# Performance work log

Measured on AMD Instinct MI355X. Metric: run time of the kernel, lower is better.

## Reference

```python
import jax, jax.numpy as jnp
import numpy as np

N = 100000   # nodes
E = 800000   # directed edges
IN = 256     # in_channels (== hidden, required by repo's vn MLP dims)
HID = 256    # hidden_channels
OUT = 40     # out_channels (arxiv classes)
EPS = 1e-5


def setup_inputs() -> dict:
    key = jax.random.key(0)
    ks = jax.random.split(key, 8)
    def nrm(k, shape, scale=0.05):
        return jax.random.normal(k, shape, dtype=jnp.float32) * scale
    return {
        "x": nrm(ks[0], (N, IN), 1.0),
        "edge_index": jax.random.randint(ks[1], (2, E), 0, N, dtype=jnp.int32),
        # GCNConv weights (PyG: x @ W, then normalized aggregation, then + bias)
        "W0": nrm(ks[2], (IN, HID)),  "b0": jnp.zeros((HID,), jnp.float32),
        "W1": nrm(ks[3], (HID, HID)), "b1": jnp.zeros((HID,), jnp.float32),
        "W2": nrm(ks[4], (HID, OUT)), "b2": jnp.zeros((OUT,), jnp.float32),
        # BatchNorm1d affine params (batch-stat math, training mode)
        "bn_g0": jnp.ones((HID,), jnp.float32), "bn_b0": jnp.zeros((HID,), jnp.float32),
        "bn_g1": jnp.ones((HID,), jnp.float32), "bn_b1": jnp.zeros((HID,), jnp.float32),
        # virtual node embedding (init to 0 per reset_parameters)
        "vn_emb": jnp.zeros((1, IN), jnp.float32),
        # mlp_vns[0]: Linear(IN,HID) + LayerNorm(HID) + ReLU
        "vn_W0": nrm(ks[5], (IN, HID)),  "vn_b0": jnp.zeros((HID,), jnp.float32),
        "ln_g0": jnp.ones((HID,), jnp.float32), "ln_b0": jnp.zeros((HID,), jnp.float32),
        # mlp_vns[1]: Linear(HID,HID) + LayerNorm(HID) + ReLU
        "vn_W1": nrm(ks[6], (HID, HID)), "vn_b1": jnp.zeros((HID,), jnp.float32),
        "ln_g1": jnp.ones((HID,), jnp.float32), "ln_b1": jnp.zeros((HID,), jnp.float32),
    }


def _forward(x, edge_index, W0, b0, W1, b1, W2, b2, bn_g0, bn_b0, bn_g1, bn_b1,
             vn_emb, vn_W0, vn_b0, ln_g0, ln_b0, vn_W1, vn_b1, ln_g1, ln_b1):
    src, dst = edge_index[0], edge_index[1]
    # GCN symmetric normalization with self-loops: deg = in-degree + 1
    deg = jax.ops.segment_sum(jnp.ones(src.shape, jnp.float32), dst, num_segments=N) + 1.0
    dis = jax.lax.rsqrt(deg)                       # deg^{-1/2}  [N]
    coef = (dis[src] * dis[dst])[:, None]          # edge norm   [E,1]
    self_coef = (dis * dis)[:, None]               # self-loop norm = deg^{-1}  [N,1]

    def gcn(h, W, b):
        h = h @ W                                             # [N, out]
        agg = jax.ops.segment_sum(h[src] * coef, dst, num_segments=N)
        return agg + h * self_coef + b

    def bn(h, g, bv):  # BatchNorm1d, batch statistics over nodes
        mu = h.mean(0)
        var = ((h - mu) ** 2).mean(0)
        return (h - mu) * jax.lax.rsqrt(var + EPS) * g + bv

    def ln(h, g, bv):  # LayerNorm over last dim
        mu = h.mean(-1, keepdims=True)
        var = ((h - mu) ** 2).mean(-1, keepdims=True)
        return (h - mu) * jax.lax.rsqrt(var + EPS) * g + bv

    vx = vn_emb                                   # [1, IN]
    # layer 0
    h = x + vx                                    # virtual-node broadcast
    h = gcn(h, W0, b0)
    h = jax.nn.relu(bn(h, bn_g0, bn_b0))          # dropout = identity (eval)
    pool = jnp.sum(h, axis=0, keepdims=True)      # global_add_pool
    vx = jax.nn.relu(ln((pool + vx) @ vn_W0 + vn_b0, ln_g0, ln_b0))
    # layer 1
    h = h + vx
    h = gcn(h, W1, b1)
    h = jax.nn.relu(bn(h, bn_g1, bn_b1))
    pool = jnp.sum(h, axis=0, keepdims=True)
    vx = jax.nn.relu(ln((pool + vx) @ vn_W1 + vn_b1, ln_g1, ln_b1))
    # layer 2 (output)
    h = h + vx
    h = gcn(h, W2, b2)
    return jax.nn.log_softmax(h, axis=-1)


def reference(x, edge_index, W0, b0, W1, b1, W2, b2, bn_g0, bn_b0, bn_g1, bn_b1,
              vn_emb, vn_W0, vn_b0, ln_g0, ln_b0, vn_W1, vn_b1, ln_g1, ln_b1):
    return _forward(x, edge_index, W0, b0, W1, b1, W2, b2, bn_g0, bn_b0, bn_g1, bn_b1,
                    vn_emb, vn_W0, vn_b0, ln_g0, ln_b0, vn_W1, vn_b1, ln_g1, ln_b1)
```

## Files before the change

kernel.cpp:

```cpp
#include <hip/hip_runtime.h>
#include <hip/hip_bf16.h>
#include <cstdint>

#define N_NODES 100000
#define N_EDGES 800000
#define CH      256
#define COUT    40
#define COUTP   48
#define EPS     1e-5f
#define SCAN_CHUNK 1024
#define NSCAN_BLK  98
#define AGG_NPW 16
#define AGG_BLOCKS 2048
#define AGG_WAVES  (AGG_BLOCKS * 4)

typedef unsigned short u16;
typedef unsigned int   u32;
typedef short s16x8 __attribute__((ext_vector_type(8)));
typedef float f32x4 __attribute__((ext_vector_type(4)));

__device__ __forceinline__ float b2f(u32 u) { return __uint_as_float(u << 16); }
__device__ __forceinline__ u16 f2b(float f) {
    u32 u = __float_as_uint(f);
    u32 r = (u + 0x7fffu + ((u >> 16) & 1u)) >> 16;
    return (u16)r;
}
__device__ __forceinline__ u32 packb(float a, float b) {
    return (u32)f2b(a) | ((u32)f2b(b) << 16);
}
__device__ __forceinline__ void unpack8(uint4 v, float* f) {
    f[0] = b2f(v.x & 0xffffu); f[1] = b2f(v.x >> 16);
    f[2] = b2f(v.y & 0xffffu); f[3] = b2f(v.y >> 16);
    f[4] = b2f(v.z & 0xffffu); f[5] = b2f(v.z >> 16);
    f[6] = b2f(v.w & 0xffffu); f[7] = b2f(v.w >> 16);
}

__global__ void k_count(const int* __restrict__ dst, int* __restrict__ counts) {
    int e = blockIdx.x * 256 + threadIdx.x;
    if (e < N_EDGES) atomicAdd(&counts[dst[e]], 1);
}

__global__ void k_scan1(const int* __restrict__ counts, int* __restrict__ partial,
                        int* __restrict__ blocksums) {
    __shared__ int sdata[256];
    int base = blockIdx.x * SCAN_CHUNK;
    int t = threadIdx.x;
    int v[4]; int s = 0;
    for (int j = 0; j < 4; j++) {
        int i = base + t * 4 + j;
        v[j] = (i < N_NODES) ? counts[i] : 0;
        s += v[j];
    }
    sdata[t] = s; __syncthreads();
    for (int off = 1; off < 256; off <<= 1) {
        int x = (t >= off) ? sdata[t - off] : 0;
        __syncthreads();
        sdata[t] += x;
        __syncthreads();
    }
    int incl = sdata[t];
    int run = incl - s;
    if (t == 255) blocksums[blockIdx.x] = incl;
    for (int j = 0; j < 4; j++) {
        int i = base + t * 4 + j;
        if (i < N_NODES) partial[i] = run;
        run += v[j];
    }
}

__global__ void k_scan3(int* __restrict__ row_start, const int* __restrict__ blocksums,
                        int* __restrict__ cursor, const int* __restrict__ counts,
                        float* __restrict__ dis) {
    __shared__ int sd[128], raw[128];
    int t = threadIdx.x;
    if (t < 128) {
        int v = (t < NSCAN_BLK) ? blocksums[t] : 0;
        sd[t] = v; raw[t] = v;
    }
    __syncthreads();
    for (int off = 1; off < 128; off <<= 1) {
        int x = (t < 128 && t >= off) ? sd[t - off] : 0;
        __syncthreads();
        if (t < 128) sd[t] += x;
        __syncthreads();
    }
    int i = blockIdx.x * 256 + t;
    if (i < N_NODES) {
        int j = i >> 10;
        int v = row_start[i] + (sd[j] - raw[j]);
        row_start[i] = v;
        cursor[i] = v;
        dis[i] = rsqrtf(1.0f + (float)counts[i]);
    }
}

__global__ void k_fill(const int* __restrict__ src, const int* __restrict__ dst,
                       int* __restrict__ cursor, int2* __restrict__ edata,
                       const float* __restrict__ dis) {
    int e = blockIdx.x * 256 + threadIdx.x;
    if (e < N_EDGES) {
        int d = dst[e], s = src[e];
        int p = atomicAdd(&cursor[d], 1);
        int2 v; v.x = s; v.y = __float_as_int(dis[s] * dis[d]);
        edata[p] = v;
    }
}

#define PREP_ZBASE (513 + COUTP)
#define PREP_ZN    (N_NODES + 2560 + 2560)
#define PREP_BLOCKS (PREP_ZBASE + (PREP_ZN + 255) / 256)
__global__ void k_prep(const float* __restrict__ W0, const float* __restrict__ W1,
                       const float* __restrict__ W2,
                       u16* __restrict__ T0, u16* __restrict__ T1, u16* __restrict__ T2,
                       const float* __restrict__ vec, float* __restrict__ v20,
                       int* __restrict__ counts, float* __restrict__ statsA,
                       float* __restrict__ statsB) {
    __shared__ float s[256];
    int b = blockIdx.x, t = threadIdx.x;
    if (b < 256) {
        T0[b * 256 + t] = f2b(W0[t * 256 + b]);
    } else if (b < 512) {
        int n = b - 256;
        T1[n * 256 + t] = f2b(W1[t * 256 + n]);
    } else if (b < 512 + COUTP) {
        int n = b - 512;
        T2[n * 256 + t] = f2b(n < COUT ? W2[t * COUT + n] : 0.f);
    } else if (b == 512 + COUTP) {
        s[t] = vec[t];
        __syncthreads();
        float acc = 0.f;
        for (int k = 0; k < 256; k++) acc += s[k] * W0[k * 256 + t];
        v20[t] = acc;
    } else {
        int idx = (b - PREP_ZBASE) * 256 + t;
        if (idx < N_NODES) counts[idx] = 0;
        else if ((idx -= N_NODES) < 2560) statsA[idx] = 0.f;
        else if ((idx -= 2560) < 2560) statsB[idx] = 0.f;
    }
}

__global__ __launch_bounds__(512) void k_gemm_f32a(const float* __restrict__ A,
                                                   const u16* __restrict__ Wt,
                                                   u16* __restrict__ Hout) {
    __shared__ u16 Bs[256 * 72];
    __shared__ u16 As[128 * 72];
    const int t = threadIdx.x;
    const int wave = t >> 6, lane = t & 63;
    const int lm = lane & 15, quad = lane >> 4;
    const int wr = wave & 1, wc = wave >> 1;
    const int m0 = blockIdx.x * 128;
    const int ar = t >> 2, as_ = (t & 3) * 16;
    const int arow = m0 + ar;
    const int brow = t >> 1, bo = (t & 1) * 32;
    const f32x4 vz = {0.f, 0.f, 0.f, 0.f};
    f32x4 acc[4][4];
    for (int m = 0; m < 4; m++)
        for (int c = 0; c < 4; c++) acc[m][c] = vz;

    for (int k0 = 0; k0 < 256; k0 += 64) {
        {
            const uint4* bsrc = (const uint4*)(Wt + brow * 256 + k0 + bo);
            uint4* bdst = (uint4*)(Bs + brow * 72 + bo);
#pragma unroll
            for (int j = 0; j < 4; j++) bdst[j] = bsrc[j];
            uint4 p0 = {0,0,0,0}, p1 = {0,0,0,0};
            if (arow < N_NODES) {
                const float4* asrc = (const float4*)(A + (size_t)arow * 256 + k0 + as_);
                float4 x0 = asrc[0], x1 = asrc[1], x2 = asrc[2], x3 = asrc[3];
                p0.x = packb(x0.x, x0.y); p0.y = packb(x0.z, x0.w);
                p0.z = packb(x1.x, x1.y); p0.w = packb(x1.z, x1.w);
                p1.x = packb(x2.x, x2.y); p1.y = packb(x2.z, x2.w);
                p1.z = packb(x3.x, x3.y); p1.w = packb(x3.z, x3.w);
            }
            uint4* adst = (uint4*)(As + ar * 72 + as_);
            adst[0] = p0; adst[1] = p1;
        }
        __syncthreads();
#pragma unroll
        for (int kk = 0; kk < 64; kk += 32) {
            s16x8 af[4], bf[4];
#pragma unroll
            for (int m = 0; m < 4; m++)
                af[m] = *(const s16x8*)(As + (wr * 64 + m * 16 + lm) * 72 + kk + quad * 8);
#pragma unroll
            for (int c = 0; c < 4; c++)
                bf[c] = *(const s16x8*)(Bs + (wc * 64 + c * 16 + lm) * 72 + kk + quad * 8);
#pragma unroll
            for (int c = 0; c < 4; c++)
#pragma unroll
                for (int m = 0; m < 4; m++)
                    acc[m][c] = __builtin_amdgcn_mfma_f32_16x16x32_bf16(af[m], bf[c], acc[m][c], 0, 0, 0);
        }
        __syncthreads();
    }
#pragma unroll
    for (int m = 0; m < 4; m++) {
#pragma unroll
        for (int c = 0; c < 4; c++) {
            int col = wc * 64 + c * 16 + lm;
#pragma unroll
            for (int i = 0; i < 4; i++) {
                int row = m0 + wr * 64 + m * 16 + quad * 4 + i;
                if (row < N_NODES) Hout[(size_t)row * 256 + col] = f2b(acc[m][c][i]);
            }
        }
    }
}

__global__ __launch_bounds__(512) void k_gemm_bn(const u16* __restrict__ A,
                                                 const float* __restrict__ stats,
                                                 const float* __restrict__ g,
                                                 const float* __restrict__ bv,
                                                 const u16* __restrict__ Wt,
                                                 u16* __restrict__ Hout,
                                                 float* __restrict__ pool) {
    __shared__ u16 Bs[256 * 72];
    __shared__ u16 As[128 * 72];
    __shared__ float ggs[256], bcs[256], pls[256];
    const int t = threadIdx.x;
    const int wave = t >> 6, lane = t & 63;
    const int lm = lane & 15, quad = lane >> 4;
    const int wr = wave & 1, wc = wave >> 1;
    const int m0 = blockIdx.x * 128;
    const int ar = t >> 2, as_ = (t & 3) * 16;
    const int arow = m0 + ar;
    const int brow = t >> 1, bo = (t & 1) * 32;
    if (t < 256) {
        const float inv = 1.0f / (float)N_NODES;
        float mu = stats[t] * inv;
        float var = stats[256 + t] * inv - mu * mu;
        float rs = rsqrtf(var + EPS);
        float gg = g[t] * rs;
        ggs[t] = gg; bcs[t] = bv[t] - mu * gg;
        pls[t] = 0.f;
    }
    __syncthreads();
    const f32x4 vz = {0.f, 0.f, 0.f, 0.f};
    f32x4 acc[4][4];
    for (int m = 0; m < 4; m++)
        for (int c = 0; c < 4; c++) acc[m][c] = vz;

    for (int k0 = 0; k0 < 256; k0 += 64) {
        {
            const uint4* bsrc = (const uint4*)(Wt + brow * 256 + k0 + bo);
            uint4* bdst = (uint4*)(Bs + brow * 72 + bo);
#pragma unroll
            for (int j = 0; j < 4; j++) bdst[j] = bsrc[j];
            float f[16];
            if (arow < N_NODES) {
                const uint4* asrc = (const uint4*)(A + (size_t)arow * 256 + k0 + as_);
                uint4 r0 = asrc[0], r1 = asrc[1];
                unpack8(r0, f); unpack8(r1, f + 8);
#pragma unroll
                for (int j = 0; j < 16; j++) {
                    int c = k0 + as_ + j;
                    f[j] = fmaxf(f[j] * ggs[c] + bcs[c], 0.f);
                }
            } else {
#pragma unroll
                for (int j = 0; j < 16; j++) f[j] = 0.f;
            }
#pragma unroll
            for (int j = 0; j < 16; j++) {
                float v = f[j];
                v += __shfl_xor(v, 4);  v += __shfl_xor(v, 8);
                v += __shfl_xor(v, 16); v += __shfl_xor(v, 32);
                if (lane < 4) atomicAdd(&pls[k0 + lane * 16 + j], v);
            }
            uint4 p0, p1;
            p0.x = packb(f[0], f[1]);   p0.y = packb(f[2], f[3]);
            p0.z = packb(f[4], f[5]);   p0.w = packb(f[6], f[7]);
            p1.x = packb(f[8], f[9]);   p1.y = packb(f[10], f[11]);
            p1.z = packb(f[12], f[13]); p1.w = packb(f[14], f[15]);
            uint4* adst = (uint4*)(As + ar * 72 + as_);
            adst[0] = p0; adst[1] = p1;
        }
        __syncthreads();
#pragma unroll
        for (int kk = 0; kk < 64; kk += 32) {
            s16x8 af[4], bf[4];
#pragma unroll
            for (int m = 0; m < 4; m++)
                af[m] = *(const s16x8*)(As + (wr * 64 + m * 16 + lm) * 72 + kk + quad * 8);
#pragma unroll
            for (int c = 0; c < 4; c++)
                bf[c] = *(const s16x8*)(Bs + (wc * 64 + c * 16 + lm) * 72 + kk + quad * 8);
#pragma unroll
            for (int c = 0; c < 4; c++)
#pragma unroll
                for (int m = 0; m < 4; m++)
                    acc[m][c] = __builtin_amdgcn_mfma_f32_16x16x32_bf16(af[m], bf[c], acc[m][c], 0, 0, 0);
        }
        __syncthreads();
    }
    if (t < 256) atomicAdd(&pool[(blockIdx.x & 7) * 256 + t], pls[t]);
#pragma unroll
    for (int m = 0; m < 4; m++) {
#pragma unroll
        for (int c = 0; c < 4; c++) {
            int col = wc * 64 + c * 16 + lm;
#pragma unroll
            for (int i = 0; i < 4; i++) {
                int row = m0 + wr * 64 + m * 16 + quad * 4 + i;
                if (row < N_NODES) Hout[(size_t)row * 256 + col] = f2b(acc[m][c][i]);
            }
        }
    }
}

__global__ __launch_bounds__(512) void k_gemm2_bn(const u16* __restrict__ A,
                                                  const float* __restrict__ stats,
                                                  const float* __restrict__ g,
                                                  const float* __restrict__ bv,
                                                  const u16* __restrict__ Wt,
                                                  u16* __restrict__ Hout,
                                                  float* __restrict__ pool) {
    __shared__ u16 Bs[48 * 72];
    __shared__ u16 As[128 * 72];
    __shared__ float ggs[256], bcs[256], pls[256];
    const int t = threadIdx.x;
    const int wave = t >> 6, lane = t & 63;
    const int lm = lane & 15, quad = lane >> 4;
    const int m0 = blockIdx.x * 128;
    const int ar = t >> 2, as_ = (t & 3) * 16;
    const int arow = m0 + ar;
    if (t < 256) {
        const float inv = 1.0f / (float)N_NODES;
        float mu = stats[t] * inv;
        float var = stats[256 + t] * inv - mu * mu;
        float rs = rsqrtf(var + EPS);
        float gg = g[t] * rs;
        ggs[t] = gg; bcs[t] = bv[t] - mu * gg;
        pls[t] = 0.f;
    }
    __syncthreads();
    const f32x4 vz = {0.f, 0.f, 0.f, 0.f};
    f32x4 acc[3]; acc[0] = vz; acc[1] = vz; acc[2] = vz;

    for (int k0 = 0; k0 < 256; k0 += 64) {
        {
            if (t < 48) {
                const uint4* bsrc = (const uint4*)(Wt + t * 256 + k0);
                uint4* bdst = (uint4*)(Bs + t * 72);
#pragma unroll
                for (int j = 0; j < 8; j++) bdst[j] = bsrc[j];
            }
            float f[16];
            if (arow < N_NODES) {
                const uint4* asrc = (const uint4*)(A + (size_t)arow * 256 + k0 + as_);
                uint4 r0 = asrc[0], r1 = asrc[1];
                unpack8(r0, f); unpack8(r1, f + 8);
#pragma unroll
                for (int j = 0; j < 16; j++) {
                    int c = k0 + as_ + j;
                    f[j] = fmaxf(f[j] * ggs[c] + bcs[c], 0.f);
                }
            } else {
#pragma unroll
                for (int j = 0; j < 16; j++) f[j] = 0.f;
            }
#pragma unroll
            for (int j = 0; j < 16; j++) {
                float v = f[j];
                v += __shfl_xor(v, 4);  v += __shfl_xor(v, 8);
                v += __shfl_xor(v, 16); v += __shfl_xor(v, 32);
                if (lane < 4) atomicAdd(&pls[k0 + lane * 16 + j], v);
            }
            uint4 p0, p1;
            p0.x = packb(f[0], f[1]);   p0.y = packb(f[2], f[3]);
            p0.z = packb(f[4], f[5]);   p0.w = packb(f[6], f[7]);
            p1.x = packb(f[8], f[9]);   p1.y = packb(f[10], f[11]);
            p1.z = packb(f[12], f[13]); p1.w = packb(f[14], f[15]);
            uint4* adst = (uint4*)(As + ar * 72 + as_);
            adst[0] = p0; adst[1] = p1;
        }
        __syncthreads();
#pragma unroll
        for (int kk = 0; kk < 64; kk += 32) {
            s16x8 af = *(const s16x8*)(As + (wave * 16 + lm) * 72 + kk + quad * 8);
#pragma unroll
            for (int c = 0; c < 3; c++) {
                s16x8 bf = *(const s16x8*)(Bs + (c * 16 + lm) * 72 + kk + quad * 8);
                acc[c] = __builtin_amdgcn_mfma_f32_16x16x32_bf16(af, bf, acc[c], 0, 0, 0);
            }
        }
        __syncthreads();
    }
    if (t < 256) atomicAdd(&pool[(blockIdx.x & 7) * 256 + t], pls[t]);
#pragma unroll
    for (int c = 0; c < 3; c++) {
        int col = c * 16 + lm;
#pragma unroll
        for (int i = 0; i < 4; i++) {
            int row = m0 + wave * 16 + quad * 4 + i;
            if (row < N_NODES) Hout[(size_t)row * COUTP + col] = f2b(acc[c][i]);
        }
    }
}

__global__ __launch_bounds__(256) void k_agg(const u16* __restrict__ H2,
                                             const int* __restrict__ row_start,
                                             const int* __restrict__ counts,
                                             const int2* __restrict__ edata,
                                             const float* __restrict__ dis,
                                             const float* __restrict__ bias,
                                             const float* __restrict__ v2,
                                             u16* __restrict__ OutB,
                                             float* __restrict__ stats) {
    __shared__ float ls[512];
    const int t = threadIdx.x, wave = t >> 6, lane = t & 63;
    const int half = lane >> 5, hl = lane & 31;
    const int ci = hl * 8;
    const float4 bbA = *(const float4*)(bias + ci);
    const float4 bbB = *(const float4*)(bias + ci + 4);
    const float4 vvA = *(const float4*)(v2 + ci);
    const float4 vvB = *(const float4*)(v2 + ci + 4);
    float s[8], q[8];
#pragma unroll
    for (int j = 0; j < 8; j++) { s[j] = 0.f; q[j] = 0.f; }

    const int gwave = blockIdx.x * 4 + wave;
    const int nid = gwave + lane * AGG_WAVES;
    const bool nv = (lane < AGG_NPW) && (nid < N_NODES);
    const int   my_rs = nv ? row_start[nid] : 0;
    const int   my_ct = nv ? counts[nid] : 0;
    const float my_dn = nv ? dis[nid] : 0.f;

    int beg = __shfl(my_rs, 0), cnt = __shfl(my_ct, 0);
    int2 my_e = {0, 0};
    if (lane < cnt) my_e = edata[beg + lane];

    for (int i = 0; i < AGG_NPW; i++) {
        const int node = gwave + i * AGG_WAVES;
        if (node >= N_NODES) break;
        const int2 cur_e = my_e;
        const int  ccnt = cnt, cbeg = beg;
        const float dn = __shfl(my_dn, i);
        const uint4 rs_ = *(const uint4*)(H2 + (size_t)node * 256 + ci);
        if (i + 1 < AGG_NPW && node + AGG_WAVES < N_NODES) {
            beg = __shfl(my_rs, i + 1);
            cnt = __shfl(my_ct, i + 1);
            int2 tmp = {0, 0};
            if (lane < cnt) tmp = edata[beg + lane];
            my_e = tmp;
        }
        const int cnt64 = ccnt < 64 ? ccnt : 64;
        const int cnt8 = (cnt64 + 7) & ~7;
        float a[8];
#pragma unroll
        for (int j = 0; j < 8; j++) a[j] = 0.f;
        float cs = 0.f;
        for (int e = 0; e < cnt8; e += 8) {
            const int   si0 = __shfl(cur_e.x, e + half);
            const int   si1 = __shfl(cur_e.x, e + 2 + half);
            const int   si2 = __shfl(cur_e.x, e + 4 + half);
            const int   si3 = __shfl(cur_e.x, e + 6 + half);
            const float cf0 = __int_as_float(__shfl(cur_e.y, e + half));
            const float cf1 = __int_as_float(__shfl(cur_e.y, e + 2 + half));
            const float cf2 = __int_as_float(__shfl(cur_e.y, e + 4 + half));
            const float cf3 = __int_as_float(__shfl(cur_e.y, e + 6 + half));
            const uint4 r0 = *(const uint4*)(H2 + (size_t)si0 * 256 + ci);
            const uint4 r1 = *(const uint4*)(H2 + (size_t)si1 * 256 + ci);
            const uint4 r2 = *(const uint4*)(H2 + (size_t)si2 * 256 + ci);
            const uint4 r3 = *(const uint4*)(H2 + (size_t)si3 * 256 + ci);
            cs += cf0 + cf1 + cf2 + cf3;
            a[0] += cf0*b2f(r0.x&0xffffu) + cf1*b2f(r1.x&0xffffu) + cf2*b2f(r2.x&0xffffu) + cf3*b2f(r3.x&0xffffu);
            a[1] += cf0*b2f(r0.x>>16)     + cf1*b2f(r1.x>>16)     + cf2*b2f(r2.x>>16)     + cf3*b2f(r3.x>>16);
            a[2] += cf0*b2f(r0.y&0xffffu) + cf1*b2f(r1.y&0xffffu) + cf2*b2f(r2.y&0xffffu) + cf3*b2f(r3.y&0xffffu);
            a[3] += cf0*b2f(r0.y>>16)     + cf1*b2f(r1.y>>16)     + cf2*b2f(r2.y>>16)     + cf3*b2f(r3.y>>16);
            a[4] += cf0*b2f(r0.z&0xffffu) + cf1*b2f(r1.z&0xffffu) + cf2*b2f(r2.z&0xffffu) + cf3*b2f(r3.z&0xffffu);
            a[5] += cf0*b2f(r0.z>>16)     + cf1*b2f(r1.z>>16)     + cf2*b2f(r2.z>>16)     + cf3*b2f(r3.z>>16);
            a[6] += cf0*b2f(r0.w&0xffffu) + cf1*b2f(r1.w&0xffffu) + cf2*b2f(r2.w&0xffffu) + cf3*b2f(r3.w&0xffffu);
            a[7] += cf0*b2f(r0.w>>16)     + cf1*b2f(r1.w>>16)     + cf2*b2f(r2.w>>16)     + cf3*b2f(r3.w>>16);
        }
        if (ccnt > 64) {
            int e2 = 64;
            for (; e2 + 2 <= ccnt; e2 += 2) {
                const int2 ed_ = edata[cbeg + e2 + half];
                const float cf = __int_as_float(ed_.y);
                const uint4 r = *(const uint4*)(H2 + (size_t)ed_.x * 256 + ci);
                cs += cf;
                a[0] += cf*b2f(r.x&0xffffu); a[1] += cf*b2f(r.x>>16);
                a[2] += cf*b2f(r.y&0xffffu); a[3] += cf*b2f(r.y>>16);
                a[4] += cf*b2f(r.z&0xffffu); a[5] += cf*b2f(r.z>>16);
                a[6] += cf*b2f(r.w&0xffffu); a[7] += cf*b2f(r.w>>16);
            }
            if (e2 < ccnt && half == 0) {
                const int2 ed_ = edata[cbeg + e2];
                const float cf = __int_as_float(ed_.y);
                const uint4 r = *(const uint4*)(H2 + (size_t)ed_.x * 256 + ci);
                cs += cf;
                a[0] += cf*b2f(r.x&0xffffu); a[1] += cf*b2f(r.x>>16);
                a[2] += cf*b2f(r.y&0xffffu); a[3] += cf*b2f(r.y>>16);
                a[4] += cf*b2f(r.z&0xffffu); a[5] += cf*b2f(r.z>>16);
                a[6] += cf*b2f(r.w&0xffffu); a[7] += cf*b2f(r.w>>16);
            }
        }
        cs += __shfl_xor(cs, 32);
#pragma unroll
        for (int j = 0; j < 8; j++) a[j] += __shfl_xor(a[j], 32);
        const float sc = dn * dn, cv = cs + sc;
        const float f0 = a[0] + sc*b2f(rs_.x&0xffffu) + cv*vvA.x + bbA.x;
        const float f1 = a[1] + sc*b2f(rs_.x>>16)     + cv*vvA.y + bbA.y;
        const float f2 = a[2] + sc*b2f(rs_.y&0xffffu) + cv*vvA.z + bbA.z;
        const float f3 = a[3] + sc*b2f(rs_.y>>16)     + cv*vvA.w + bbA.w;
        const float f4 = a[4] + sc*b2f(rs_.z&0xffffu) + cv*vvB.x + bbB.x;
        const float f5 = a[5] + sc*b2f(rs_.z>>16)     + cv*vvB.y + bbB.y;
        const float f6 = a[6] + sc*b2f(rs_.w&0xffffu) + cv*vvB.z + bbB.z;
        const float f7 = a[7] + sc*b2f(rs_.w>>16)     + cv*vvB.w + bbB.w;
        if (half == 0) {
            uint4 o;
            o.x = packb(f0, f1); o.y = packb(f2, f3);
            o.z = packb(f4, f5); o.w = packb(f6, f7);
            *(uint4*)(OutB + (size_t)node * 256 + ci) = o;
        }
        s[0] += f0; q[0] += f0*f0;  s[1] += f1; q[1] += f1*f1;
        s[2] += f2; q[2] += f2*f2;  s[3] += f3; q[3] += f3*f3;
        s[4] += f4; q[4] += f4*f4;  s[5] += f5; q[5] += f5*f5;
        s[6] += f6; q[6] += f6*f6;  s[7] += f7; q[7] += f7*f7;
    }
    ls[t] = 0.f; ls[256 + t] = 0.f;
    __syncthreads();
    if (half == 0) {
#pragma unroll
        for (int j = 0; j < 8; j++) {
            atomicAdd(&ls[ci + j], s[j]);
            atomicAdd(&ls[256 + ci + j], q[j]);
        }
    }
    __syncthreads();
    atomicAdd(&stats[t], ls[t]);
    atomicAdd(&stats[256 + t], ls[256 + t]);
}

__global__ void k_vx(const float* __restrict__ pool, const float* __restrict__ vx_old,
                     const float* __restrict__ vnW, const float* __restrict__ vnb,
                     const float* __restrict__ lng, const float* __restrict__ lnb,
                     float* __restrict__ vx_new,
                     const float* __restrict__ Wnext, int ncn, int npn,
                     float* __restrict__ v2n) {
    __shared__ float s[256];
    __shared__ float red[256];
    int t = threadIdx.x;
    float pv = 0.f;
#pragma unroll
    for (int r = 0; r < 8; r++) pv += pool[r * 256 + t];
    s[t] = pv + vx_old[t];
    __syncthreads();
    float y = vnb[t];
    for (int k = 0; k < 256; k++) y += s[k] * vnW[k * 256 + t];
    red[t] = y; __syncthreads();
    for (int off = 128; off > 0; off >>= 1) {
        if (t < off) red[t] += red[t + off];
        __syncthreads();
    }
    float mu = red[0] * (1.f / 256.f);
    __syncthreads();
    float d = y - mu;
    red[t] = d * d; __syncthreads();
    for (int off = 128; off > 0; off >>= 1) {
        if (t < off) red[t] += red[t + off];
        __syncthreads();
    }
    float var = red[0] * (1.f / 256.f);
    float v = fmaxf(d * rsqrtf(var + EPS) * lng[t] + lnb[t], 0.f);
    vx_new[t] = v;
    __syncthreads();
    s[t] = v;
    __syncthreads();
    float acc = 0.f;
    if (t < ncn) {
        for (int k = 0; k < 256; k++) acc += s[k] * Wnext[k * ncn + t];
    }
    if (t < npn) v2n[t] = acc;
}

__global__ __launch_bounds__(256) void k_agg2(const u16* __restrict__ H2,
                                              const int* __restrict__ row_start,
                                              const int* __restrict__ counts,
                                              const int2* __restrict__ edata,
                                              const float* __restrict__ dis,
                                              const float* __restrict__ bias,
                                              const float* __restrict__ v2,
                                              float* __restrict__ OutF) {
    const int t = threadIdx.x, wave = t >> 6, lane = t & 63;
    const int half = lane >> 5, hl = lane & 31;
    const bool gact = hl < 24;
    const bool cact = hl < 20;
    const int c0 = 2 * hl;
    float bb0 = 0.f, bb1 = 0.f, vv0 = 0.f, vv1 = 0.f;
    if (cact) {
        float2 bv = *(const float2*)(bias + c0); bb0 = bv.x; bb1 = bv.y;
        float2 vvv = *(const float2*)(v2 + c0);  vv0 = vvv.x; vv1 = vvv.y;
    }
    const int nbase = blockIdx.x * 16 + wave * 4;
    for (int i = 0; i < 4; i++) {
        const int node = nbase + i;
        const int beg = row_start[node], cnt = counts[node];
        const float dn = dis[node];
        float a0 = 0.f, a1 = 0.f, cs = 0.f;
        int e = half;
        for (; e + 6 < cnt; e += 8) {
            int2 ea = edata[beg+e],   eb = edata[beg+e+2];
            int2 ec = edata[beg+e+4], ed = edata[beg+e+6];
            float ca = __int_as_float(ea.y), cb = __int_as_float(eb.y);
            float cc = __int_as_float(ec.y), cd = __int_as_float(ed.y);
            u32 ra = 0, rb = 0, rc = 0, rd = 0;
            if (gact) {
                ra = *(const u32*)(H2 + (size_t)ea.x * COUTP + c0);
                rb = *(const u32*)(H2 + (size_t)eb.x * COUTP + c0);
                rc = *(const u32*)(H2 + (size_t)ec.x * COUTP + c0);
                rd = *(const u32*)(H2 + (size_t)ed.x * COUTP + c0);
            }
            cs += ca + cb + cc + cd;
            a0 += ca*b2f(ra&0xffffu) + cb*b2f(rb&0xffffu) + cc*b2f(rc&0xffffu) + cd*b2f(rd&0xffffu);
            a1 += ca*b2f(ra>>16)     + cb*b2f(rb>>16)     + cc*b2f(rc>>16)     + cd*b2f(rd>>16);
        }
        for (; e < cnt; e += 2) {
            int2 ea = edata[beg+e];
            float ca = __int_as_float(ea.y);
            u32 ra = gact ? *(const u32*)(H2 + (size_t)ea.x * COUTP + c0) : 0u;
            cs += ca;
            a0 += ca*b2f(ra&0xffffu); a1 += ca*b2f(ra>>16);
        }
        a0 += __shfl_xor(a0, 32);
        a1 += __shfl_xor(a1, 32);
        cs += __shfl_xor(cs, 32);
        const float sc = dn * dn;
        u32 rs_ = gact ? *(const u32*)(H2 + (size_t)node * COUTP + c0) : 0u;
        float h0 = a0 + sc*b2f(rs_&0xffffu) + (cs+sc)*vv0 + bb0;
        float h1 = a1 + sc*b2f(rs_>>16)     + (cs+sc)*vv1 + bb1;
        float m = cact ? fmaxf(h0, h1) : -3.0e38f;
#pragma unroll
        for (int off = 16; off > 0; off >>= 1) m = fmaxf(m, __shfl_xor(m, off));
        float ex = cact ? (expf(h0 - m) + expf(h1 - m)) : 0.f;
        float se = ex;
#pragma unroll
        for (int off = 16; off > 0; off >>= 1) se += __shfl_xor(se, off);
        float lg = logf(se);
        if (cact && half == 0) {
            float2 o = {h0 - m - lg, h1 - m - lg};
            *(float2*)(OutF + (size_t)node * COUT + c0) = o;
        }
    }
}

extern "C" void kernel_launch(void* const* d_in, const int* in_sizes, int n_in,
                              void* d_out, int out_size, void* d_ws, size_t ws_size,
                              hipStream_t stream) {
    const float* x   = (const float*)d_in[0];
    const int*   ei  = (const int*)d_in[1];
    const int*   esrc = ei;
    const int*   edst = ei + N_EDGES;
    const float* W0 = (const float*)d_in[2];  const float* b0 = (const float*)d_in[3];
    const float* W1 = (const float*)d_in[4];  const float* b1 = (const float*)d_in[5];
    const float* W2 = (const float*)d_in[6];  const float* b2 = (const float*)d_in[7];
    const float* bg0 = (const float*)d_in[8]; const float* bb0 = (const float*)d_in[9];
    const float* bg1 = (const float*)d_in[10]; const float* bb1 = (const float*)d_in[11];
    const float* vn_emb = (const float*)d_in[12];
    const float* vW0 = (const float*)d_in[13]; const float* vb0 = (const float*)d_in[14];
    const float* lg0 = (const float*)d_in[15]; const float* lb0 = (const float*)d_in[16];
    const float* vW1 = (const float*)d_in[17]; const float* vb1 = (const float*)d_in[18];
    const float* lg1 = (const float*)d_in[19]; const float* lb1 = (const float*)d_in[20];

    char* w = (char*)d_ws;
    auto alloc = [&](size_t bytes) { void* p = (void*)w; w += ((bytes + 255) / 256) * 256; return p; };
    u16* H2    = (u16*)alloc((size_t)N_NODES * 256 * 2);
    u16* OutB  = (u16*)alloc((size_t)N_NODES * 256 * 2);
    int2* edata = (int2*)alloc((size_t)N_EDGES * 8);
    int* counts = (int*)alloc((size_t)N_NODES * 4);
    int* rowst  = (int*)alloc((size_t)N_NODES * 4);
    int* cursor = (int*)alloc((size_t)N_NODES * 4);
    float* dis  = (float*)alloc((size_t)N_NODES * 4);
    u16* Wtb0 = (u16*)alloc(256 * 256 * 2);
    u16* Wtb1 = (u16*)alloc(256 * 256 * 2);
    u16* Wt2b = (u16*)alloc(COUTP * 256 * 2);
    int* scanblk = (int*)alloc(128 * 4);
    float* statsA = (float*)alloc(2560 * 4);
    float* statsB = (float*)alloc(2560 * 4);
    float* vxA = (float*)alloc(256 * 4);
    float* vxB = (float*)alloc(256 * 4);
    float* v20 = (float*)alloc(256 * 4);
    float* v21 = (float*)alloc(256 * 4);
    float* v22 = (float*)alloc(64 * 4);
    (void)ws_size; (void)in_sizes; (void)n_in; (void)out_size;

    k_prep<<<PREP_BLOCKS, 256, 0, stream>>>(W0, W1, W2, Wtb0, Wtb1, Wt2b,
                                            vn_emb, v20, counts, statsA, statsB);
    k_count<<<(N_EDGES + 255) / 256, 256, 0, stream>>>(edst, counts);
    k_scan1<<<NSCAN_BLK, 256, 0, stream>>>(counts, rowst, scanblk);
    k_scan3<<<(N_NODES + 255) / 256, 256, 0, stream>>>(rowst, scanblk, cursor, counts, dis);
    k_fill<<<(N_EDGES + 255) / 256, 256, 0, stream>>>(esrc, edst, cursor, edata, dis);

    const int gemmblk = (N_NODES + 127) / 128;

    k_gemm_f32a<<<gemmblk, 512, 0, stream>>>(x, Wtb0, H2);
    k_agg<<<AGG_BLOCKS, 256, 0, stream>>>(H2, rowst, counts, edata, dis, b0, v20, OutB, statsA);
    k_gemm_bn<<<gemmblk, 512, 0, stream>>>(OutB, statsA, bg0, bb0, Wtb1, H2, statsA + 512);
    k_vx<<<1, 256, 0, stream>>>(statsA + 512, vn_emb, vW0, vb0, lg0, lb0, vxA, W1, 256, 256, v21);
    k_agg<<<AGG_BLOCKS, 256, 0, stream>>>(H2, rowst, counts, edata, dis, b1, v21, OutB, statsB);
    k_gemm2_bn<<<gemmblk, 512, 0, stream>>>(OutB, statsB, bg1, bb1, Wt2b, H2, statsB + 512);
    k_vx<<<1, 256, 0, stream>>>(statsB + 512, vxA, vW1, vb1, lg1, lb1, vxB, W2, COUT, COUTP, v22);
    k_agg2<<<N_NODES / 16, 256, 0, stream>>>(H2, rowst, counts, edata, dis, b2, v22, (float*)d_out);
}
```

Measured before the change: 719.4 us.

## Load GEMM B fragments directly from global memory instead of staging in LDS

The three GEMM kernels no longer copy the transposed weight tile into shared memory each k-step. Each lane now reads its B fragment straight from global memory, relying on cache hits since the weights are small and shared by every block. This removes the LDS stores and frees shared memory, which may raise occupancy, at the cost of more global/L2 traffic per MFMA. The padded output width grows from 48 to 64 to match four 16-column MFMA tiles, and the final aggregation only loads the 40 real columns.

```diff
diff --git a/kernel.cpp b/kernel.cpp
--- a/kernel.cpp
+++ b/kernel.cpp
@@ -6,7 +6,7 @@
 #define N_EDGES 800000
 #define CH      256
 #define COUT    40
-#define COUTP   48
+#define COUTP   64
 #define EPS     1e-5f
 #define SCAN_CHUNK 1024
 #define NSCAN_BLK  98
@@ -142,7 +142,6 @@
 __global__ __launch_bounds__(512) void k_gemm_f32a(const float* __restrict__ A,
                                                    const u16* __restrict__ Wt,
                                                    u16* __restrict__ Hout) {
-    __shared__ u16 Bs[256 * 72];
     __shared__ u16 As[128 * 72];
     const int t = threadIdx.x;
     const int wave = t >> 6, lane = t & 63;
@@ -151,7 +150,7 @@
     const int m0 = blockIdx.x * 128;
     const int ar = t >> 2, as_ = (t & 3) * 16;
     const int arow = m0 + ar;
-    const int brow = t >> 1, bo = (t & 1) * 32;
+    const u16* bbase = Wt + (wc * 64 + lm) * 256 + quad * 8;
     const f32x4 vz = {0.f, 0.f, 0.f, 0.f};
     f32x4 acc[4][4];
     for (int m = 0; m < 4; m++)
@@ -159,10 +158,6 @@
 
     for (int k0 = 0; k0 < 256; k0 += 64) {
         {
-            const uint4* bsrc = (const uint4*)(Wt + brow * 256 + k0 + bo);
-            uint4* bdst = (uint4*)(Bs + brow * 72 + bo);
-#pragma unroll
-            for (int j = 0; j < 4; j++) bdst[j] = bsrc[j];
             uint4 p0 = {0,0,0,0}, p1 = {0,0,0,0};
             if (arow < N_NODES) {
                 const float4* asrc = (const float4*)(A + (size_t)arow * 256 + k0 + as_);
@@ -184,7 +179,7 @@
                 af[m] = *(const s16x8*)(As + (wr * 64 + m * 16 + lm) * 72 + kk + quad * 8);
 #pragma unroll
             for (int c = 0; c < 4; c++)
-                bf[c] = *(const s16x8*)(Bs + (wc * 64 + c * 16 + lm) * 72 + kk + quad * 8);
+                bf[c] = *(const s16x8*)(bbase + c * 16 * 256 + k0 + kk);
 #pragma unroll
             for (int c = 0; c < 4; c++)
 #pragma unroll
@@ -214,7 +209,6 @@
                                                  const u16* __restrict__ Wt,
                                                  u16* __restrict__ Hout,
                                                  float* __restrict__ pool) {
-    __shared__ u16 Bs[256 * 72];
     __shared__ u16 As[128 * 72];
     __shared__ float ggs[256], bcs[256], pls[256];
     const int t = threadIdx.x;
@@ -224,7 +218,7 @@
     const int m0 = blockIdx.x * 128;
     const int ar = t >> 2, as_ = (t & 3) * 16;
     const int arow = m0 + ar;
-    const int brow = t >> 1, bo = (t & 1) * 32;
+    const u16* bbase = Wt + (wc * 64 + lm) * 256 + quad * 8;
     if (t < 256) {
         const float inv = 1.0f / (float)N_NODES;
         float mu = stats[t] * inv;
@@ -242,10 +236,6 @@
 
     for (int k0 = 0; k0 < 256; k0 += 64) {
         {
-            const uint4* bsrc = (const uint4*)(Wt + brow * 256 + k0 + bo);
-            uint4* bdst = (uint4*)(Bs + brow * 72 + bo);
-#pragma unroll
-            for (int j = 0; j < 4; j++) bdst[j] = bsrc[j];
             float f[16];
             if (arow < N_NODES) {
                 const uint4* asrc = (const uint4*)(A + (size_t)arow * 256 + k0 + as_);
@@ -284,7 +274,7 @@
                 af[m] = *(const s16x8*)(As + (wr * 64 + m * 16 + lm) * 72 + kk + quad * 8);
 #pragma unroll
             for (int c = 0; c < 4; c++)
-                bf[c] = *(const s16x8*)(Bs + (wc * 64 + c * 16 + lm) * 72 + kk + quad * 8);
+                bf[c] = *(const s16x8*)(bbase + c * 16 * 256 + k0 + kk);
 #pragma unroll
             for (int c = 0; c < 4; c++)
 #pragma unroll
@@ -315,7 +305,6 @@
                                                   const u16* __restrict__ Wt,
                                                   u16* __restrict__ Hout,
                                                   float* __restrict__ pool) {
-    __shared__ u16 Bs[48 * 72];
     __shared__ u16 As[128 * 72];
     __shared__ float ggs[256], bcs[256], pls[256];
     const int t = threadIdx.x;
@@ -324,6 +313,7 @@
     const int m0 = blockIdx.x * 128;
     const int ar = t >> 2, as_ = (t & 3) * 16;
     const int arow = m0 + ar;
+    const u16* bbase = Wt + lm * 256 + quad * 8;
     if (t < 256) {
         const float inv = 1.0f / (float)N_NODES;
         float mu = stats[t] * inv;
@@ -335,16 +325,10 @@
     }
     __syncthreads();
     const f32x4 vz = {0.f, 0.f, 0.f, 0.f};
-    f32x4 acc[3]; acc[0] = vz; acc[1] = vz; acc[2] = vz;
+    f32x4 acc[4]; acc[0] = vz; acc[1] = vz; acc[2] = vz; acc[3] = vz;
 
     for (int k0 = 0; k0 < 256; k0 += 64) {
         {
-            if (t < 48) {
-                const uint4* bsrc = (const uint4*)(Wt + t * 256 + k0);
-                uint4* bdst = (uint4*)(Bs + t * 72);
-#pragma unroll
-                for (int j = 0; j < 8; j++) bdst[j] = bsrc[j];
-            }
             float f[16];
             if (arow < N_NODES) {
                 const uint4* asrc = (const uint4*)(A + (size_t)arow * 256 + k0 + as_);
@@ -379,8 +363,8 @@
         for (int kk = 0; kk < 64; kk += 32) {
             s16x8 af = *(const s16x8*)(As + (wave * 16 + lm) * 72 + kk + quad * 8);
 #pragma unroll
-            for (int c = 0; c < 3; c++) {
-                s16x8 bf = *(const s16x8*)(Bs + (c * 16 + lm) * 72 + kk + quad * 8);
+            for (int c = 0; c < 4; c++) {
+                s16x8 bf = *(const s16x8*)(bbase + c * 16 * 256 + k0 + kk);
                 acc[c] = __builtin_amdgcn_mfma_f32_16x16x32_bf16(af, bf, acc[c], 0, 0, 0);
             }
         }
@@ -388,7 +372,7 @@
     }
     if (t < 256) atomicAdd(&pool[(blockIdx.x & 7) * 256 + t], pls[t]);
 #pragma unroll
-    for (int c = 0; c < 3; c++) {
+    for (int c = 0; c < 4; c++) {
         int col = c * 16 + lm;
 #pragma unroll
         for (int i = 0; i < 4; i++) {
@@ -585,7 +569,6 @@
                                               float* __restrict__ OutF) {
     const int t = threadIdx.x, wave = t >> 6, lane = t & 63;
     const int half = lane >> 5, hl = lane & 31;
-    const bool gact = hl < 24;
     const bool cact = hl < 20;
     const int c0 = 2 * hl;
     float bb0 = 0.f, bb1 = 0.f, vv0 = 0.f, vv1 = 0.f;
@@ -606,7 +589,7 @@
             float ca = __int_as_float(ea.y), cb = __int_as_float(eb.y);
             float cc = __int_as_float(ec.y), cd = __int_as_float(ed.y);
             u32 ra = 0, rb = 0, rc = 0, rd = 0;
-            if (gact) {
+            if (cact) {
                 ra = *(const u32*)(H2 + (size_t)ea.x * COUTP + c0);
                 rb = *(const u32*)(H2 + (size_t)eb.x * COUTP + c0);
                 rc = *(const u32*)(H2 + (size_t)ec.x * COUTP + c0);
@@ -619,7 +602,7 @@
         for (; e < cnt; e += 2) {
             int2 ea = edata[beg+e];
             float ca = __int_as_float(ea.y);
-            u32 ra = gact ? *(const u32*)(H2 + (size_t)ea.x * COUTP + c0) : 0u;
+            u32 ra = cact ? *(const u32*)(H2 + (size_t)ea.x * COUTP + c0) : 0u;
             cs += ca;
             a0 += ca*b2f(ra&0xffffu); a1 += ca*b2f(ra>>16);
         }
@@ -627,7 +610,7 @@
         a1 += __shfl_xor(a1, 32);
         cs += __shfl_xor(cs, 32);
         const float sc = dn * dn;
-        u32 rs_ = gact ? *(const u32*)(H2 + (size_t)node * COUTP + c0) : 0u;
+        u32 rs_ = cact ? *(const u32*)(H2 + (size_t)node * COUTP + c0) : 0u;
         float h0 = a0 + sc*b2f(rs_&0xffffu) + (cs+sc)*vv0 + bb0;
         float h1 = a1 + sc*b2f(rs_>>16)     + (cs+sc)*vv1 + bb1;
         float m = cact ? fmaxf(h0, h1) : -3.0e38f;
@@ -682,7 +665,7 @@
     float* vxB = (float*)alloc(256 * 4);
     float* v20 = (float*)alloc(256 * 4);
     float* v21 = (float*)alloc(256 * 4);
-    float* v22 = (float*)alloc(64 * 4);
+    float* v22 = (float*)alloc(COUTP * 4);
     (void)ws_size; (void)in_sizes; (void)n_in; (void)out_size;
 
     k_prep<<<PREP_BLOCKS, 256, 0, stream>>>(W0, W1, W2, Wtb0, Wtb1, Wt2b,
```

After: 743.2 us. 3.3% more time.
